# Performance work log

Hardware: AMD Instinct MI355X
Metric: run time of the kernel (lower is better)

The kernel has to match this reference:

```python
import jax, jax.numpy as jnp
import numpy as np

B, N, K, D, H = 32, 4096, 8, 256, 512
ITERS = 3
LN_EPS = 1e-5  # torch LayerNorm default; self.eps is unused in forward


def _ln(x, g, b):
    m = jnp.mean(x, axis=-1, keepdims=True)
    v = jnp.mean(jnp.square(x - m), axis=-1, keepdims=True)
    return (x - m) * jax.lax.rsqrt(v + LN_EPS) * g + b


def setup_inputs() -> dict:
    key = jax.random.key(0)
    ks = jax.random.split(key, 16)
    s = 0.02
    return {
        "inputs": jax.random.normal(ks[0], (B, N, D), jnp.float32),
        "slots_init": jax.random.normal(ks[1], (B, K, D), jnp.float32),
        "ln_in_g": jnp.ones((D,), jnp.float32), "ln_in_b": jnp.zeros((D,), jnp.float32),
        "ln_s_g": jnp.ones((D,), jnp.float32), "ln_s_b": jnp.zeros((D,), jnp.float32),
        "ln_ff_g": jnp.ones((D,), jnp.float32), "ln_ff_b": jnp.zeros((D,), jnp.float32),
        "Wk": s * jax.random.normal(ks[2], (D, D), jnp.float32), "bk": jnp.zeros((D,), jnp.float32),
        "Wq": s * jax.random.normal(ks[3], (D, D), jnp.float32), "bq": jnp.zeros((D,), jnp.float32),
        "Wv": s * jax.random.normal(ks[4], (D, D), jnp.float32), "bv": jnp.zeros((D,), jnp.float32),
        "W_ih": s * jax.random.normal(ks[5], (3 * D, D), jnp.float32),
        "b_ih": jnp.zeros((3 * D,), jnp.float32),
        "W_hh": s * jax.random.normal(ks[6], (3 * D, D), jnp.float32),
        "b_hh": jnp.zeros((3 * D,), jnp.float32),
        "W1": s * jax.random.normal(ks[7], (H, D), jnp.float32), "b1": jnp.zeros((H,), jnp.float32),
        "W2": s * jax.random.normal(ks[8], (D, H), jnp.float32), "b2": jnp.zeros((D,), jnp.float32),
    }


def _gru_cell(x, h, W_ih, b_ih, W_hh, b_hh):
    # PyTorch GRUCell: gates in order r, z, n
    gi = x @ W_ih.T + b_ih  # [*, 3D]
    gh = h @ W_hh.T + b_hh
    ir, iz, inn = jnp.split(gi, 3, axis=-1)
    hr, hz, hn = jnp.split(gh, 3, axis=-1)
    r = jax.nn.sigmoid(ir + hr)
    z = jax.nn.sigmoid(iz + hz)
    n = jnp.tanh(inn + r * hn)
    return (1.0 - z) * n + z * h


def reference(inputs, slots_init, ln_in_g, ln_in_b, ln_s_g, ln_s_b, ln_ff_g, ln_ff_b,
              Wk, bk, Wq, bq, Wv, bv, W_ih, b_ih, W_hh, b_hh, W1, b1, W2, b2):
    d = inputs.shape[-1]
    x = _ln(inputs, ln_in_g, ln_in_b)  # [B,N,D]
    # k, v depend only on x; hoisted out of the loop (same math as source)
    k = x @ Wk.T + bk                  # project_inputs
    v = x @ Wv.T + bv                  # project_v
    scale = 1.0 / jnp.sqrt(jnp.asarray(d, inputs.dtype))
    slots = slots_init
    for _ in range(ITERS):
        slots_prev = slots
        q = _ln(slots, ln_s_g, ln_s_b) @ Wq.T + bq          # [B,K,D]
        attn_logits = jnp.einsum('bkd,bnd->bkn', q, k) * scale
        # competitive softmax over the SLOT axis (dim=1), not keys
        attn = jax.nn.softmax(attn_logits, axis=1)          # [B,K,N]
        updates = jnp.einsum('bkn,bnd->bkd', attn, v)
        slots = _gru_cell(updates, slots_prev, W_ih, b_ih, W_hh, b_hh)
        hdd = jax.nn.relu(_ln(slots, ln_ff_g, ln_ff_b) @ W1.T + b1)
        slots = slots + hdd @ W2.T + b2
    return slots
```

## Files before the change

kernel.cpp:

```cpp
#include <hip/hip_runtime.h>
#include <hip/hip_bf16.h>
#include <cstddef>
#include <cstdint>

#define BB 32
#define NN 4096
#define KK 8
#define DD 256
#define HH 512
#define LN_EPS 1e-5f
#define SCALE 0.0625f
#define NCHUNK 32

__device__ __forceinline__ float wave_sum(float v) {
#pragma unroll
  for (int off = 32; off >= 1; off >>= 1) v += __shfl_xor(v, off);
  return v;
}

__device__ __forceinline__ float sigmoidf_(float x) { return 1.0f / (1.0f + __expf(-x)); }

__device__ __forceinline__ uint pk2bf(float x, float y) {
  __hip_bfloat16 hx = __float2bfloat16(x), hy = __float2bfloat16(y);
  return (uint)*(ushort*)&hx | ((uint)*(ushort*)&hy << 16);
}

#define OFF_G   0
#define OFF_W1  393216
#define OFF_W2  524288
#define OFF_WV  655360
#define OFF_WQ  720896
#define OFF_WK  786432
#define WB_ELEMS 851968

#define G_PRE (BB * KK)
#define G_W2B (512 * 11)
#define G_SETUP (G_PRE + G_W2B + 1)

__device__ __forceinline__ float dotp4(uint2 w, float4 s) {
  return __uint_as_float(w.x << 16) * s.x + __uint_as_float(w.x & 0xffff0000u) * s.y +
         __uint_as_float(w.y << 16) * s.z + __uint_as_float(w.y & 0xffff0000u) * s.w;
}

template <int OUT, int KL>
__device__ __forceinline__ float gemv_p(const ushort* __restrict__ wt, int j, int kb,
                                        const float* __restrict__ src) {
  const uint2* p = (const uint2*)(wt + ((size_t)(kb >> 2) * OUT + j) * 4);
  float a = 0.0f;
#pragma unroll 16
  for (int e = 0; e < KL / 4; ++e) {
    uint2 w = p[(size_t)e * OUT];
    float4 s = *(const float4*)(src + kb + e * 4);
    a += dotp4(w, s);
  }
  return a;
}

__global__ __launch_bounds__(256) void k_setup(
    const float* __restrict__ Wih, const float* __restrict__ Whh,
    const float* __restrict__ W1, const float* __restrict__ W2,
    const float* __restrict__ Wv, const float* __restrict__ Wq,
    const float* __restrict__ Wk, ushort* __restrict__ wb,
    const float* __restrict__ slots, const float* __restrict__ gs, const float* __restrict__ bs,
    const float* __restrict__ bq, const float* __restrict__ bk,
    const float* __restrict__ gi, const float* __restrict__ bi,
    const float* __restrict__ bv, float* __restrict__ bvw,
    float* __restrict__ qk, float* __restrict__ qb) {
  int blk = blockIdx.x;
  if (blk < G_PRE) {
    int row = blk;
    int t = threadIdx.x;
    int wid = t >> 6, lane = t & 63;
    __shared__ float lns[DD];
    __shared__ float qs[DD];
    __shared__ float rb[8];
    float sv = slots[(size_t)row * DD + t];
    float s = wave_sum(sv);
    float s2 = wave_sum(sv * sv);
    if (lane == 0) { rb[wid] = s; rb[4 + wid] = s2; }
    __syncthreads();
    float tot = rb[0] + rb[1] + rb[2] + rb[3];
    float tot2 = rb[4] + rb[5] + rb[6] + rb[7];
    float m = tot * (1.0f / DD);
    float var = tot2 * (1.0f / DD) - m * m;
    float rs = rsqrtf(var + LN_EPS);
    lns[t] = (sv - m) * rs * gs[t] + bs[t];
    __syncthreads();
    float acc = 0.0f;
    const float4* wr = (const float4*)(Wq + (size_t)t * DD);
#pragma unroll 4
    for (int e4 = 0; e4 < DD / 4; ++e4) {
      float4 w = wr[e4];
      float4 l = ((const float4*)lns)[e4];
      acc += w.x * l.x + w.y * l.y + w.z * l.z + w.w * l.w;
    }
    qs[t] = acc + bq[t];
    __syncthreads();
    float a2 = 0.0f;
    for (int d = 0; d < DD; ++d) a2 = fmaf(qs[d], Wk[(size_t)d * DD + t], a2);
    float a2S = SCALE * a2;
    qk[(size_t)row * DD + t] = a2S * gi[t];
    float pb = wave_sum(qs[t] * bk[t]);
    float pb2 = wave_sum(a2S * bi[t]);
    __syncthreads();
    if (lane == 0) { rb[wid] = pb; rb[4 + wid] = pb2; }
    __syncthreads();
    if (t == 0) qb[row] = SCALE * (rb[0] + rb[1] + rb[2] + rb[3]) + rb[4] + rb[5] + rb[6] + rb[7];
  } else if (blk < G_PRE + G_W2B) {
    int q2 = blk - G_PRE;
    int m = q2 >> 9;
    int idx = (q2 & 511) * 256 + threadIdx.x;
    const int sizes[11] = {65536, 65536, 65536, 65536, 65536, 65536, 131072, 131072, 65536, 65536, 65536};
    const int offs[11] = {OFF_G, OFF_G + 65536, OFF_G + 131072, OFF_G + 196608, OFF_G + 262144,
                          OFF_G + 327680, OFF_W1, OFF_W2, OFF_WV, OFF_WQ, OFF_WK};
    if (idx >= sizes[m]) return;
    int K = (m == 7) ? 512 : 256;
    int OUT = (m == 6) ? 512 : 256;
    int k = idx % K, j = idx / K;
    float v;
    switch (m) {
      case 0: case 1: case 2: v = Wih[((size_t)(m * 256 + j)) * 256 + k]; break;
      case 3: case 4: case 5: v = Whh[((size_t)((m - 3) * 256 + j)) * 256 + k]; break;
      case 6: v = W1[(size_t)j * 256 + k]; break;
      case 7: v = W2[(size_t)j * 512 + k]; break;
      case 8: v = Wv[(size_t)j * 256 + k] * gi[k]; break;
      case 9: v = Wq[(size_t)j * 256 + k]; break;
      default: v = Wk[(size_t)k * 256 + j]; break;
    }
    __hip_bfloat16 h = __float2bfloat16(v);
    wb[(size_t)offs[m] + (size_t)(k >> 2) * OUT * 4 + j * 4 + (k & 3)] = *(ushort*)&h;
  } else {
    int t = threadIdx.x;
    float a = bv[t];
    const float4* wr = (const float4*)(Wv + (size_t)t * DD);
    const float4* bb = (const float4*)bi;
#pragma unroll 4
    for (int e4 = 0; e4 < DD / 4; ++e4) {
      float4 w = wr[e4];
      float4 x = bb[e4];
      a += w.x * x.x + w.y * x.y + w.z * x.z + w.w * x.w;
    }
    bvw[t] = a;
  }
}

template <int DO_LN>
__global__ __launch_bounds__(256, 4) void k_attn_t(const ushort* __restrict__ xb_in,
                                                   ushort* __restrict__ xb_out,
                                                   const float* __restrict__ inp,
                                                   const float* __restrict__ qk,
                                                   const float* __restrict__ qb,
                                                   float* __restrict__ uxp,
                                                   float* __restrict__ sap) {
  typedef __attribute__((ext_vector_type(8))) short short8;
  typedef __attribute__((ext_vector_type(4))) float f32x4;
  union V16 { uint4 u; short8 s; ushort us[8]; };

  __shared__ __align__(16) ushort q_l[16 * 256];
  __shared__ __align__(16) ushort xbuf[32 * 256];
  __shared__ __align__(16) float scr[4 * 512];

  int t = threadIdx.x, wid = t >> 6, lane = t & 63;
  int bI = blockIdx.x >> 5, c = blockIdx.x & 31;
  int lm = lane & 15, g = lane >> 4;
  char* xwB = (char*)xbuf;
  char* qB = (char*)q_l;

  {
    const float* qkb = qk + (size_t)bI * (KK * DD);
    int p = t >> 3, e7 = t & 7;
#pragma unroll 1
    for (int s = 0; s < 8; ++s) {
      float qv = qkb[s * 256 + t];
      __hip_bfloat16 hb = __float2bfloat16(qv);
      float lo = qv - __bfloat162float(hb);
      __hip_bfloat16 lb = __float2bfloat16(lo);
      *(ushort*)(qB + s * 512 + (((p + s) & 31) << 4) + e7 * 2) = *(ushort*)&hb;
      *(ushort*)(qB + (s + 8) * 512 + (((p + s + 8) & 31) << 4) + e7 * 2) = *(ushort*)&lb;
    }
  }
  float qbv = qb[bI * 8 + (lane & 7)];

  f32x4 avacc[4];
#pragma unroll
  for (int i = 0; i < 4; ++i) avacc[i] = (f32x4){0.0f, 0.0f, 0.0f, 0.0f};
  float stot = 0.0f;

#pragma unroll 1
  for (int tt = 0; tt < 4; ++tt) {
    int row0 = c * 128 + tt * 32;

    if (DO_LN) {
      __syncthreads();
      int q8 = t & 7, rr = t >> 3;
      const float* rp = inp + ((size_t)bI * NN + row0 + rr) * DD + q8 * 4;
      float4 cur[8];
#pragma unroll
      for (int i = 0; i < 8; ++i) cur[i] = *(const float4*)(rp + i * 32);
      float s1 = 0.0f, s2 = 0.0f;
#pragma unroll
      for (int i = 0; i < 8; ++i) {
        s1 += cur[i].x + cur[i].y + cur[i].z + cur[i].w;
        s2 += cur[i].x * cur[i].x + cur[i].y * cur[i].y + cur[i].z * cur[i].z + cur[i].w * cur[i].w;
      }
      s1 += __shfl_xor(s1, 1); s2 += __shfl_xor(s2, 1);
      s1 += __shfl_xor(s1, 2); s2 += __shfl_xor(s2, 2);
      s1 += __shfl_xor(s1, 4); s2 += __shfl_xor(s2, 4);
      float m = s1 * (1.0f / DD);
      float var = s2 * (1.0f / DD) - m * m;
      float rs = rsqrtf(var + LN_EPS);
      int pb = q8 >> 1, hb8 = (q8 & 1) * 8;
#pragma unroll
      for (int i = 0; i < 8; ++i) {
        uint2 wv;
        wv.x = pk2bf((cur[i].x - m) * rs, (cur[i].y - m) * rs);
        wv.y = pk2bf((cur[i].z - m) * rs, (cur[i].w - m) * rs);
        *(uint2*)(xwB + ((4 * i + pb) << 9) + (rr << 4) + hb8) = wv;
      }
      __syncthreads();
      ushort* xbt = xb_out + ((size_t)bI * NN + row0) * DD;
#pragma unroll
      for (int i = 0; i < 4; ++i)
        *(uint4*)((char*)xbt + i * 4096 + t * 16) = *(const uint4*)(xwB + i * 4096 + t * 16);
    } else {
      __syncthreads();
      const ushort* srcb = xb_in + ((size_t)bI * NN + row0) * DD;
#pragma unroll
      for (int i = 0; i < 4; ++i) {
        __builtin_amdgcn_global_load_lds(
            (__attribute__((address_space(1))) void*)(srcb + i * 2048 + wid * 512 + lane * 8),
            (__attribute__((address_space(3))) void*)(xbuf + i * 2048 + wid * 512), 16, 0, 0);
      }
      asm volatile("s_waitcnt vmcnt(0)" ::: "memory");
      __syncthreads();
    }

    f32x4 p0 = (f32x4){0.0f, 0.0f, 0.0f, 0.0f}, p1 = (f32x4){0.0f, 0.0f, 0.0f, 0.0f};
#pragma unroll
    for (int kx = 0; kx < 2; ++kx) {
      int ch = (2 * wid + kx) * 4 + g;
      V16 qf, x0, x1;
      qf.u = *(const uint4*)(qB + (lm << 9) + (((ch + lm) & 31) << 4));
      x0.u = *(const uint4*)(xwB + (ch << 9) + (lm << 4));
      x1.u = *(const uint4*)(xwB + (ch << 9) + ((lm + 16) << 4));
      p0 = __builtin_amdgcn_mfma_f32_16x16x32_bf16(x0.s, qf.s, p0, 0, 0, 0);
      p1 = __builtin_amdgcn_mfma_f32_16x16x32_bf16(x1.s, qf.s, p1, 0, 0, 0);
    }
    *(f32x4*)&scr[wid * 512 + lane * 8] = p0;
    *(f32x4*)&scr[wid * 512 + lane * 8 + 4] = p1;
    __syncthreads();

    f32x4 s0 = (f32x4){0.0f, 0.0f, 0.0f, 0.0f}, s1v = (f32x4){0.0f, 0.0f, 0.0f, 0.0f};
#pragma unroll
    for (int w2 = 0; w2 < 4; ++w2) {
      s0 += *(const f32x4*)&scr[w2 * 512 + lane * 8];
      s1v += *(const f32x4*)&scr[w2 * 512 + lane * 8 + 4];
    }

    float a0[4], a1[4];
    {
      float lv0[4], lv1[4], mx0[4], mx1[4], ss0[4], ss1[4];
#pragma unroll
      for (int r = 0; r < 4; ++r) {
        lv0[r] = s0[r] + __shfl_xor(s0[r], 8) + qbv;
        lv1[r] = s1v[r] + __shfl_xor(s1v[r], 8) + qbv;
        mx0[r] = lv0[r]; mx1[r] = lv1[r];
      }
#pragma unroll
      for (int off = 1; off <= 4; off <<= 1) {
#pragma unroll
        for (int r = 0; r < 4; ++r) {
          mx0[r] = fmaxf(mx0[r], __shfl_xor(mx0[r], off));
          mx1[r] = fmaxf(mx1[r], __shfl_xor(mx1[r], off));
        }
      }
#pragma unroll
      for (int r = 0; r < 4; ++r) {
        a0[r] = __expf(lv0[r] - mx0[r]);
        a1[r] = __expf(lv1[r] - mx1[r]);
        ss0[r] = a0[r]; ss1[r] = a1[r];
      }
#pragma unroll
      for (int off = 1; off <= 4; off <<= 1) {
#pragma unroll
        for (int r = 0; r < 4; ++r) {
          ss0[r] += __shfl_xor(ss0[r], off);
          ss1[r] += __shfl_xor(ss1[r], off);
        }
      }
#pragma unroll
      for (int r = 0; r < 4; ++r) {
        a0[r] *= __frcp_rn(ss0[r]);
        a1[r] *= __frcp_rn(ss1[r]);
      }
    }
    float sacc = 0.0f;
#pragma unroll
    for (int r = 0; r < 4; ++r) sacc += a0[r] + a1[r];
    sacc += __shfl_xor(sacc, 16);
    sacc += __shfl_xor(sacc, 32);
    stot += sacc;

    bool lop = (lane & 8) != 0;
    V16 au;
    {
      float t8[8];
#pragma unroll
      for (int e = 0; e < 8; ++e) {
        float av = (e < 4) ? a0[e] : a1[e - 4];
        if (lop) {
          __hip_bfloat16 hb = __float2bfloat16(av);
          av = av - __bfloat162float(hb);
        }
        t8[e] = av;
      }
      au.u = make_uint4(pk2bf(t8[0], t8[1]), pk2bf(t8[2], t8[3]),
                        pk2bf(t8[4], t8[5]), pk2bf(t8[6], t8[7]));
    }

#pragma unroll
    for (int cc = 0; cc < 4; ++cc) {
      int dc = 4 * wid + cc;
      int d = dc * 16 + lm, dch = d >> 3, d7b = (d & 7) * 2;
      int r0 = 4 * g, r2 = 16 + 4 * g;
      const char* pl = xwB + (dch << 9) + d7b;
      V16 bu;
      bu.u.x = (uint)*(const ushort*)(pl + ((r0 + 0) << 4)) |
               ((uint)*(const ushort*)(pl + ((r0 + 1) << 4)) << 16);
      bu.u.y = (uint)*(const ushort*)(pl + ((r0 + 2) << 4)) |
               ((uint)*(const ushort*)(pl + ((r0 + 3) << 4)) << 16);
      bu.u.z = (uint)*(const ushort*)(pl + ((r2 + 0) << 4)) |
               ((uint)*(const ushort*)(pl + ((r2 + 1) << 4)) << 16);
      bu.u.w = (uint)*(const ushort*)(pl + ((r2 + 2) << 4)) |
               ((uint)*(const ushort*)(pl + ((r2 + 3) << 4)) << 16);
      avacc[cc] = __builtin_amdgcn_mfma_f32_16x16x32_bf16(au.s, bu.s, avacc[cc], 0, 0, 0);
    }
  }

  size_t obase = ((size_t)(bI * NCHUNK + c)) * (KK * DD);
#pragma unroll
  for (int cc = 0; cc < 4; ++cc) {
#pragma unroll
    for (int r = 0; r < 4; ++r) {
      float v = avacc[cc][r];
      float o = v + __shfl_xor(v, 32);
      if (lane < 32) uxp[obase + (g * 4 + r) * 256 + (4 * wid + cc) * 16 + lm] = o;
    }
  }
  if (wid == 0 && lane < 8) sap[((size_t)(bI * NCHUNK + c)) * KK + lane] = stot;
}

__global__ __launch_bounds__(1024) void k_fused(const float* __restrict__ slots_in,
                                                const float* __restrict__ uxp,
                                                const float* __restrict__ sap,
                                                const ushort* __restrict__ wb,
                                                const float* __restrict__ bv,
                                                const float* __restrict__ bih, const float* __restrict__ bhh,
                                                const float* __restrict__ gff, const float* __restrict__ bff,
                                                const float* __restrict__ b1, const float* __restrict__ b2,
                                                const float* __restrict__ gs, const float* __restrict__ bs,
                                                const float* __restrict__ bq, const float* __restrict__ bk,
                                                const float* __restrict__ gi, const float* __restrict__ bi,
                                                float* __restrict__ dst,
                                                float* __restrict__ qk_out,
                                                float* __restrict__ qb_out,
                                                int last) {
  const ushort* WG = wb + OFF_G;
  const ushort* W1p = wb + OFF_W1;
  const ushort* W2p = wb + OFF_W2;
  const ushort* WVp = wb + OFF_WV;
  const ushort* WQp = wb + OFF_WQ;
  const ushort* WKp = wb + OFF_WK;

  __shared__ float ux_s[DD], h_s[DD], upd_s[DD], hn_s[DD], ln_s[DD];
  __shared__ float g_s[6][DD];
  __shared__ float hdd_s[HH];
  __shared__ float tmp4_s[4][DD];
  __shared__ float red_s[16];
  __shared__ float sA_s;
  float* tmpH = &tmp4_s[0][0];

  int t = threadIdx.x, d = t & 255, qr = t >> 8;
  int wid = t >> 6, lane = t & 63;
  int r = blockIdx.x, b = r >> 3, k = r & 7;

  {
    const float* p = uxp + (((size_t)(b * NCHUNK + qr * 8)) * KK + k) * DD + d;
    float s = 0.0f;
#pragma unroll
    for (int i = 0; i < 8; ++i) s += p[(size_t)i * KK * DD];
    tmp4_s[qr][d] = s;
  }
  if (t < 256) h_s[t] = slots_in[(size_t)r * DD + t];
  if (t >= 960) {
    int c = t - 960;
    float v = (c < NCHUNK) ? sap[((size_t)(b * NCHUNK + c)) * KK + k] : 0.0f;
    v = wave_sum(v);
    if (lane == 0) sA_s = v;
  }
  __syncthreads();
  if (t < 256) ux_s[t] = tmp4_s[0][t] + tmp4_s[1][t] + tmp4_s[2][t] + tmp4_s[3][t];
  __syncthreads();

  tmp4_s[qr][d] = gemv_p<256, 64>(WVp, d, qr * 64, ux_s);
  __syncthreads();
  if (t < 256) upd_s[t] = tmp4_s[0][t] + tmp4_s[1][t] + tmp4_s[2][t] + tmp4_s[3][t] + bv[t] * sA_s;
  __syncthreads();

  {
    int g = qr;
    const float* src = (g < 3) ? upd_s : h_s;
    float a = gemv_p<256, 256>(WG + (size_t)g * 65536, d, 0, src);
    g_s[g][d] = a + ((g < 3) ? bih[g * 256 + d] : bhh[d]);
    if (t < 512) {
      int g2 = 4 + (t >> 8), j2 = t & 255;
      float a2 = gemv_p<256, 256>(WG + (size_t)g2 * 65536, j2, 0, h_s);
      g_s[g2][j2] = a2 + bhh[(g2 - 3) * 256 + j2];
    }
  }
  __syncthreads();
  if (t < 256) {
    float rr = sigmoidf_(g_s[0][t] + g_s[3][t]);
    float zz = sigmoidf_(g_s[1][t] + g_s[4][t]);
    float nn = tanhf(g_s[2][t] + rr * g_s[5][t]);
    hn_s[t] = (1.0f - zz) * nn + zz * h_s[t];
  }
  __syncthreads();

  if (t < 256) {
    float v = hn_s[t];
    float sm = wave_sum(v), sq = wave_sum(v * v);
    if (lane == 0) { red_s[wid] = sm; red_s[8 + wid] = sq; }
  }
  __syncthreads();
  if (t < 256) {
    float v = hn_s[t];
    float tot = red_s[0] + red_s[1] + red_s[2] + red_s[3];
    float tot2 = red_s[8] + red_s[9] + red_s[10] + red_s[11];
    float m = tot * (1.0f / DD);
    float var = tot2 * (1.0f / DD) - m * m;
    float rs = rsqrtf(var + LN_EPS);
    ln_s[t] = (v - m) * rs * gff[t] + bff[t];
  }
  __syncthreads();

  {
    int o = t & 511, kh = t >> 9;
    tmpH[kh * 512 + o] = gemv_p<512, 128>(W1p, o, kh * 128, ln_s);
  }
  __syncthreads();
  if (t < 512) hdd_s[t] = fmaxf(tmpH[t] + tmpH[512 + t] + b1[t], 0.0f);
  __syncthreads();

  tmp4_s[qr][d] = gemv_p<256, 128>(W2p, d, qr * 128, hdd_s);
  __syncthreads();
  if (t < 256) {
    float o = hn_s[t] + tmp4_s[0][t] + tmp4_s[1][t] + tmp4_s[2][t] + tmp4_s[3][t] + b2[t];
    dst[(size_t)r * DD + t] = o;
    ux_s[t] = o;
  }
  __syncthreads();

  if (!last) {
    if (t < 256) {
      float v = ux_s[t];
      float sm = wave_sum(v), sq = wave_sum(v * v);
      if (lane == 0) { red_s[wid] = sm; red_s[8 + wid] = sq; }
    }
    __syncthreads();
    if (t < 256) {
      float v = ux_s[t];
      float tot = red_s[0] + red_s[1] + red_s[2] + red_s[3];
      float tot2 = red_s[8] + red_s[9] + red_s[10] + red_s[11];
      float m = tot * (1.0f / DD);
      float var = tot2 * (1.0f / DD) - m * m;
      float rs = rsqrtf(var + LN_EPS);
      ln_s[t] = (v - m) * rs * gs[t] + bs[t];
    }
    __syncthreads();
    tmp4_s[qr][d] = gemv_p<256, 64>(WQp, d, qr * 64, ln_s);
    __syncthreads();
    if (t < 256) {
      float qv = tmp4_s[0][t] + tmp4_s[1][t] + tmp4_s[2][t] + tmp4_s[3][t] + bq[t];
      upd_s[t] = qv;
      float sb = wave_sum(qv * bk[t]);
      if (lane == 0) red_s[wid] = sb;
    }
    __syncthreads();
    {
      float a = gemv_p<256, 64>(WKp, d, qr * 64, upd_s);
      tmp4_s[qr][d] = a;
    }
    __syncthreads();
    if (t < 256) {
      float qkv = SCALE * (tmp4_s[0][t] + tmp4_s[1][t] + tmp4_s[2][t] + tmp4_s[3][t]);
      qk_out[(size_t)r * DD + t] = qkv * gi[t];
      float pb2 = wave_sum(qkv * bi[t]);
      if (lane == 0) red_s[8 + wid] = pb2;
    }
    __syncthreads();
    if (t == 0) qb_out[r] = SCALE * (red_s[0] + red_s[1] + red_s[2] + red_s[3]) +
                            red_s[8] + red_s[9] + red_s[10] + red_s[11];
  }
}

extern "C" void kernel_launch(void* const* d_in, const int* in_sizes, int n_in,
                              void* d_out, int out_size, void* d_ws, size_t ws_size,
                              hipStream_t stream) {
  const float* inputs = (const float*)d_in[0];
  const float* slots_init = (const float*)d_in[1];
  const float* ln_in_g = (const float*)d_in[2];
  const float* ln_in_b = (const float*)d_in[3];
  const float* ln_s_g = (const float*)d_in[4];
  const float* ln_s_b = (const float*)d_in[5];
  const float* ln_ff_g = (const float*)d_in[6];
  const float* ln_ff_b = (const float*)d_in[7];
  const float* Wk = (const float*)d_in[8];
  const float* bk = (const float*)d_in[9];
  const float* Wq = (const float*)d_in[10];
  const float* bq = (const float*)d_in[11];
  const float* Wv = (const float*)d_in[12];
  const float* bv = (const float*)d_in[13];
  const float* Wih = (const float*)d_in[14];
  const float* bih = (const float*)d_in[15];
  const float* Whh = (const float*)d_in[16];
  const float* bhh = (const float*)d_in[17];
  const float* W1 = (const float*)d_in[18];
  const float* b1 = (const float*)d_in[19];
  const float* W2 = (const float*)d_in[20];
  const float* b2 = (const float*)d_in[21];
  float* outp = (float*)d_out;

  char* w = (char*)d_ws;
  ushort* xb = (ushort*)w;       w += (size_t)BB * NN * DD * 2;
  float* qk = (float*)w;         w += (size_t)BB * KK * DD * 4;
  float* qb = (float*)w;         w += (size_t)BB * KK * 4;
  float* uxp = (float*)w;        w += (size_t)BB * NCHUNK * KK * DD * 4;
  float* sap = (float*)w;        w += (size_t)BB * NCHUNK * KK * 4;
  float* slots_ws = (float*)w;   w += (size_t)BB * KK * DD * 4;
  ushort* wb = (ushort*)w;       w += (size_t)WB_ELEMS * 2;
  float* bvw = (float*)w;        w += (size_t)DD * 4;

  k_setup<<<G_SETUP, 256, 0, stream>>>(Wih, Whh, W1, W2, Wv, Wq, Wk, wb,
                                       slots_init, ln_s_g, ln_s_b, bq, bk,
                                       ln_in_g, ln_in_b, bv, bvw, qk, qb);

  for (int it = 0; it < 3; ++it) {
    if (it == 0)
      k_attn_t<1><<<BB * NCHUNK, 256, 0, stream>>>(nullptr, xb, inputs, qk, qb, uxp, sap);
    else
      k_attn_t<0><<<BB * NCHUNK, 256, 0, stream>>>(xb, nullptr, nullptr, qk, qb, uxp, sap);
    const float* sin = (it == 0) ? slots_init : slots_ws;
    float* dst = (it == 2) ? outp : slots_ws;
    k_fused<<<BB * KK, 1024, 0, stream>>>(sin, uxp, sap, wb,
                                          bvw, bih, bhh, ln_ff_g, ln_ff_b, b1, b2,
                                          ln_s_g, ln_s_b, bq, bk, ln_in_g, ln_in_b,
                                          dst, qk, qb, (it == 2) ? 1 : 0);
  }
}
```

Measured before the change: 230.8 us.

## Double-buffer x tiles via async LDS loads and drop cross-wave logit reduction

Double-buffers the bf16 x tile in shared memory so the next 32-row tile is prefetched with global_load_lds while the current tile is computed, replacing the load-wait-barrier per iteration. Each wave now computes the full K=256 logits dot product itself (8 MFMA steps) instead of splitting K across waves and reducing through a shared scratch buffer, removing a barrier and the LDS round trip. This trades redundant MFMA work across the four waves for fewer syncs, and doubles the x-tile LDS footprint, which may affect occupancy.

```diff
diff --git a/kernel.cpp b/kernel.cpp
--- a/kernel.cpp
+++ b/kernel.cpp
@@ -157,13 +157,11 @@
   union V16 { uint4 u; short8 s; ushort us[8]; };
 
   __shared__ __align__(16) ushort q_l[16 * 256];
-  __shared__ __align__(16) ushort xbuf[32 * 256];
-  __shared__ __align__(16) float scr[4 * 512];
+  __shared__ __align__(16) ushort xtile[2][32 * 256];
 
   int t = threadIdx.x, wid = t >> 6, lane = t & 63;
   int bI = blockIdx.x >> 5, c = blockIdx.x & 31;
   int lm = lane & 15, g = lane >> 4;
-  char* xwB = (char*)xbuf;
   char* qB = (char*)q_l;
 
   {
@@ -186,8 +184,19 @@
   for (int i = 0; i < 4; ++i) avacc[i] = (f32x4){0.0f, 0.0f, 0.0f, 0.0f};
   float stot = 0.0f;
 
+  if (!DO_LN) {
+    const ushort* s0 = xb_in + ((size_t)bI * NN + c * 128) * DD;
+#pragma unroll
+    for (int i = 0; i < 4; ++i) {
+      __builtin_amdgcn_global_load_lds(
+          (__attribute__((address_space(1))) void*)(s0 + i * 2048 + wid * 512 + lane * 8),
+          (__attribute__((address_space(3))) void*)(xtile[0] + i * 2048 + wid * 512), 16, 0, 0);
+    }
+  }
+
 #pragma unroll 1
   for (int tt = 0; tt < 4; ++tt) {
+    char* xwB = (char*)xtile[tt & 1];
     int row0 = c * 128 + tt * 32;
 
     if (DO_LN) {
@@ -215,7 +224,7 @@
         uint2 wv;
         wv.x = pk2bf((cur[i].x - m) * rs, (cur[i].y - m) * rs);
         wv.y = pk2bf((cur[i].z - m) * rs, (cur[i].w - m) * rs);
-        *(uint2*)(xwB + ((4 * i + pb) << 9) + (rr << 4) + hb8) = wv;
+        *(uint2*)(xwB + ((4 * i + pb) << 9) + ((t >> 3) << 4) + hb8) = wv;
       }
       __syncthreads();
       ushort* xbt = xb_out + ((size_t)bI * NN + row0) * DD;
@@ -223,38 +232,33 @@
       for (int i = 0; i < 4; ++i)
         *(uint4*)((char*)xbt + i * 4096 + t * 16) = *(const uint4*)(xwB + i * 4096 + t * 16);
     } else {
-      __syncthreads();
-      const ushort* srcb = xb_in + ((size_t)bI * NN + row0) * DD;
-#pragma unroll
-      for (int i = 0; i < 4; ++i) {
-        __builtin_amdgcn_global_load_lds(
-            (__attribute__((address_space(1))) void*)(srcb + i * 2048 + wid * 512 + lane * 8),
-            (__attribute__((address_space(3))) void*)(xbuf + i * 2048 + wid * 512), 16, 0, 0);
-      }
-      asm volatile("s_waitcnt vmcnt(0)" ::: "memory");
-      __syncthreads();
-    }
-
-    f32x4 p0 = (f32x4){0.0f, 0.0f, 0.0f, 0.0f}, p1 = (f32x4){0.0f, 0.0f, 0.0f, 0.0f};
-#pragma unroll
-    for (int kx = 0; kx < 2; ++kx) {
-      int ch = (2 * wid + kx) * 4 + g;
+      asm volatile("s_waitcnt vmcnt(0) lgkmcnt(0)" ::: "memory");
+      __builtin_amdgcn_sched_barrier(0);
+      __builtin_amdgcn_s_barrier();
+      __builtin_amdgcn_sched_barrier(0);
+      if (tt < 3) {
+        const ushort* sn = xb_in + ((size_t)bI * NN + c * 128 + (tt + 1) * 32) * DD;
+        ushort* db = xtile[(tt + 1) & 1];
+#pragma unroll
+        for (int i = 0; i < 4; ++i) {
+          __builtin_amdgcn_global_load_lds(
+              (__attribute__((address_space(1))) void*)(sn + i * 2048 + wid * 512 + lane * 8),
+              (__attribute__((address_space(3))) void*)(db + i * 2048 + wid * 512), 16, 0, 0);
+        }
+      }
+    }
+
+    int rA = lm, rB = lm + 16;
+    f32x4 ac0 = {}, ac1 = {};
+#pragma unroll
+    for (int kk = 0; kk < 8; ++kk) {
       V16 qf, x0, x1;
+      int ch = kk * 4 + g;
       qf.u = *(const uint4*)(qB + (lm << 9) + (((ch + lm) & 31) << 4));
-      x0.u = *(const uint4*)(xwB + (ch << 9) + (lm << 4));
-      x1.u = *(const uint4*)(xwB + (ch << 9) + ((lm + 16) << 4));
-      p0 = __builtin_amdgcn_mfma_f32_16x16x32_bf16(x0.s, qf.s, p0, 0, 0, 0);
-      p1 = __builtin_amdgcn_mfma_f32_16x16x32_bf16(x1.s, qf.s, p1, 0, 0, 0);
-    }
-    *(f32x4*)&scr[wid * 512 + lane * 8] = p0;
-    *(f32x4*)&scr[wid * 512 + lane * 8 + 4] = p1;
-    __syncthreads();
-
-    f32x4 s0 = (f32x4){0.0f, 0.0f, 0.0f, 0.0f}, s1v = (f32x4){0.0f, 0.0f, 0.0f, 0.0f};
-#pragma unroll
-    for (int w2 = 0; w2 < 4; ++w2) {
-      s0 += *(const f32x4*)&scr[w2 * 512 + lane * 8];
-      s1v += *(const f32x4*)&scr[w2 * 512 + lane * 8 + 4];
+      x0.u = *(const uint4*)(xwB + (ch << 9) + (rA << 4));
+      x1.u = *(const uint4*)(xwB + (ch << 9) + (rB << 4));
+      ac0 = __builtin_amdgcn_mfma_f32_16x16x32_bf16(x0.s, qf.s, ac0, 0, 0, 0);
+      ac1 = __builtin_amdgcn_mfma_f32_16x16x32_bf16(x1.s, qf.s, ac1, 0, 0, 0);
     }
 
     float a0[4], a1[4];
@@ -262,8 +266,8 @@
       float lv0[4], lv1[4], mx0[4], mx1[4], ss0[4], ss1[4];
 #pragma unroll
       for (int r = 0; r < 4; ++r) {
-        lv0[r] = s0[r] + __shfl_xor(s0[r], 8) + qbv;
-        lv1[r] = s1v[r] + __shfl_xor(s1v[r], 8) + qbv;
+        lv0[r] = ac0[r] + __shfl_xor(ac0[r], 8) + qbv;
+        lv1[r] = ac1[r] + __shfl_xor(ac1[r], 8) + qbv;
         mx0[r] = lv0[r]; mx1[r] = lv1[r];
       }
 #pragma unroll
```

Measured after the change: 231.6 us. Within noise of the previous version (+0.4%).
